# Kernel optimization log

Measured on AMD Instinct MI355X. Metric: run time of the kernel, lower is better.

The kernel has to match this reference:

```python
import jax, jax.numpy as jnp
import numpy as np

NUM_CLASSES = 80
STRIDES = (8, 16, 32)


def bce_logits(x, t):
    # numerically stable BCEWithLogits, reduction='none'
    return jnp.maximum(x, 0.) - x * t + jnp.log1p(jnp.exp(-jnp.abs(x)))


def decode_level(feat, stride):
    # feat: [B, C, H, W] -> decoded [B, HW, C], grid x/y [HW], strides [HW]
    B, C, H, W = feat.shape
    out = feat.reshape(B, C, H * W).transpose(0, 2, 1)  # [B, HW, C]
    yv, xv = jnp.meshgrid(jnp.arange(H), jnp.arange(W), indexing='ij')
    grid = jnp.stack([xv, yv], axis=-1).reshape(-1, 2).astype(feat.dtype)  # [HW, 2]
    xy = (out[..., :2] + grid[None]) * stride
    wh = jnp.exp(out[..., 2:4]) * stride
    out = jnp.concatenate([xy, wh, out[..., 4:]], axis=-1)
    return out, grid[:, 0], grid[:, 1], jnp.full((H * W,), float(stride), feat.dtype)


def pairwise_iou_cxcywh(g, p):
    # g: [G,4] gt boxes, p: [A,4] pred boxes (cx,cy,w,h) -> [G,A]
    tl = jnp.maximum(g[:, None, :2] - g[:, None, 2:] * 0.5, p[None, :, :2] - p[None, :, 2:] * 0.5)
    br = jnp.minimum(g[:, None, :2] + g[:, None, 2:] * 0.5, p[None, :, :2] + p[None, :, 2:] * 0.5)
    area_g = g[:, 2] * g[:, 3]
    area_p = p[:, 2] * p[:, 3]
    en = jnp.all(tl < br, axis=-1)
    inter = jnp.prod(br - tl, axis=-1) * en
    return inter / (area_g[:, None] + area_p[None, :] - inter + 1e-16)


def simota_assign(gt_boxes, gt_cls, bbox_p, cls_p, obj_p, xc, yc, strides):
    # per-image SimOTA label assignment (masked, jit-friendly)
    # gt_boxes [G,4], gt_cls [G] int, bbox_p [A,4], cls_p [A,C], obj_p [A,1]
    G = gt_boxes.shape[0]
    A = bbox_p.shape[0]
    gl = gt_boxes[:, 0:1] - 0.5 * gt_boxes[:, 2:3]
    gr = gt_boxes[:, 0:1] + 0.5 * gt_boxes[:, 2:3]
    gt_ = gt_boxes[:, 1:2] - 0.5 * gt_boxes[:, 3:4]
    gb = gt_boxes[:, 1:2] + 0.5 * gt_boxes[:, 3:4]
    in_box = (xc[None] > gl) & (xc[None] < gr) & (yc[None] > gt_) & (yc[None] < gb)  # [G,A]
    r = 2.5 * strides[None]
    in_ctr = ((xc[None] > gt_boxes[:, 0:1] - r) & (xc[None] < gt_boxes[:, 0:1] + r)
              & (yc[None] > gt_boxes[:, 1:2] - r) & (yc[None] < gt_boxes[:, 1:2] + r))
    geom = in_box | in_ctr
    anchor_ok = jnp.any(geom, axis=0)        # fg_mask candidate anchors [A]
    in_both = in_box & in_ctr                # [G,A]

    ious = pairwise_iou_cxcywh(gt_boxes, bbox_p)            # [G,A]
    ious = jnp.where(anchor_ok[None], ious, 0.)
    iou_cost = -jnp.log(ious + 1e-8)

    eps = 1e-8
    p = jnp.sqrt(jax.nn.sigmoid(cls_p) * jax.nn.sigmoid(obj_p))  # [A,C]
    logp = jnp.log(p + eps)
    log1mp = jnp.log(1. - p + eps)
    base = -jnp.sum(log1mp, axis=-1)                              # [A]
    sel = (logp - log1mp)[:, gt_cls]                              # [A,G]
    cls_cost = base[None, :] - sel.T                              # [G,A] = BCE(p, onehot).sum(-1)

    cost = cls_cost + 3.0 * iou_cost + 100000.0 * (~in_both) + 1e9 * (~anchor_ok[None])

    n_cand = min(10, A)
    topk_ious = jax.lax.top_k(ious, n_cand)[0]                    # [G,10]
    dyn_k = jnp.maximum(jnp.sum(topk_ious, axis=1).astype(jnp.int32), 1)  # [G]
    rank = jnp.argsort(jnp.argsort(cost, axis=1), axis=1)         # rank of each anchor per gt
    matching = (rank < dyn_k[:, None]) & anchor_ok[None]          # [G,A] bool

    am = jnp.sum(matching, axis=0)                                # anchors matched to >1 gt
    argmin_g = jnp.argmin(cost, axis=0)                           # [A]
    best = jnp.arange(G)[:, None] == argmin_g[None]               # [G,A]
    matching = jnp.where(am[None] > 1, best, matching)

    fg = jnp.any(matching, axis=0)                                # [A]
    matched_gt = jnp.argmax(matching, axis=0)                     # [A]
    pred_iou = jnp.sum(matching * ious, axis=0)                   # [A]
    cls_t = jax.nn.one_hot(gt_cls[matched_gt], NUM_CLASSES, dtype=bbox_p.dtype) * pred_iou[:, None]
    reg_t = gt_boxes[matched_gt]                                  # [A,4]
    return fg, cls_t, reg_t


def iou_elem(p, t):
    # elementwise IoU between matched pred/target boxes (cxcywh), IOUloss 'iou'
    tl = jnp.maximum(p[..., :2] - p[..., 2:] * 0.5, t[..., :2] - t[..., 2:] * 0.5)
    br = jnp.minimum(p[..., :2] + p[..., 2:] * 0.5, t[..., :2] + t[..., 2:] * 0.5)
    ap = p[..., 2] * p[..., 3]
    ag = t[..., 2] * t[..., 3]
    en = jnp.all(tl < br, axis=-1).astype(p.dtype)
    ai = jnp.prod(br - tl, axis=-1) * en
    return ai / (ap + ag - ai + 1e-16)


def yolo_loss(feat8, feat16, feat32, labels):
    outs, xs, ys, ss = [], [], [], []
    for feat, s in zip((feat8, feat16, feat32), STRIDES):
        o, x, y, st = decode_level(feat, s)
        outs.append(o); xs.append(x); ys.append(y); ss.append(st)
    outputs = jnp.concatenate(outs, axis=1)            # [B, A, 5+C]
    x_shifts = jnp.concatenate(xs)
    y_shifts = jnp.concatenate(ys)
    strides = jnp.concatenate(ss)
    xc = (x_shifts + 0.5) * strides                    # anchor centers [A]
    yc = (y_shifts + 0.5) * strides

    bbox_preds = outputs[..., :4]
    obj_preds = outputs[..., 4]
    cls_preds = outputs[..., 5:5 + NUM_CLASSES]

    labels_sg = jax.lax.stop_gradient(labels)
    gt_boxes = labels_sg[..., :4]
    gt_cls = labels_sg[..., 4].astype(jnp.int32)

    # assignment is @torch.no_grad in the original -> stop_gradient on its inputs
    fg, cls_t, reg_t = jax.vmap(simota_assign, in_axes=(0, 0, 0, 0, 0, None, None, None))(
        gt_boxes, gt_cls,
        jax.lax.stop_gradient(bbox_preds),
        jax.lax.stop_gradient(cls_preds),
        jax.lax.stop_gradient(outputs[..., 4:5]),
        xc, yc, strides)

    fg_f = fg.astype(outputs.dtype)                    # [B, A]
    iou = iou_elem(bbox_preds, reg_t)                  # [B, A]
    loss_iou = jnp.sum(fg_f * (1. - iou ** 2))
    loss_obj = jnp.sum(bce_logits(obj_preds, fg_f))
    loss_cls = jnp.sum(fg_f[..., None] * bce_logits(cls_preds, cls_t))
    num_fg = jnp.maximum(jnp.sum(fg_f), 1.)
    loss = (5.0 * loss_iou + 0.1 * loss_obj + loss_cls) / num_fg
    return loss


def setup_inputs() -> dict:
    key = jax.random.key(0)
    k1, k2, k3, k4, k5, k6, k7 = jax.random.split(key, 7)
    B, G = 32, 30
    feat8 = jax.random.normal(k1, (B, 85, 80, 80), jnp.float32)
    feat16 = jax.random.normal(k2, (B, 85, 40, 40), jnp.float32)
    feat32 = jax.random.normal(k3, (B, 85, 20, 20), jnp.float32)
    cx = jax.random.uniform(k4, (B, G, 1), jnp.float32, 60., 580.)
    cy = jax.random.uniform(k5, (B, G, 1), jnp.float32, 60., 580.)
    wh = jax.random.uniform(k6, (B, G, 2), jnp.float32, 20., 150.)
    cls = jax.random.randint(k7, (B, G, 1), 0, NUM_CLASSES).astype(jnp.float32)
    labels = jnp.concatenate([cx, cy, wh, cls], axis=-1)   # [B, G, 5] = cx,cy,w,h,cls
    return {"feat8": feat8, "feat16": feat16, "feat32": feat32, "labels": labels}


def reference(feat8, feat16, feat32, labels):
    return yolo_loss(feat8, feat16, feat32, labels)
```

## Files before the change

### kernel.cpp

```cpp
#include <hip/hip_runtime.h>
#include <cstdint>
#include <cstddef>

#define NB 32
#define NG 30
#define NA 8400
#define NC 80
#define SELB 512
#define MGRIDX 33
#define NBLK (MGRIDX * NB)
#define LCAP 128
#define DCAP 2304
#define NITER 17

typedef unsigned long long u64;

struct Params {
  const float* f8; const float* f16; const float* f32; const float* lab;
  float*    bbox;
  float*    objlog;
  float*    po;
  float*    base_;
  unsigned* gbits;
  unsigned* obits;
  unsigned* mmask;
  unsigned* dcount;
  unsigned* dlist;
  float*    part;
  float*    out;
};

__device__ __forceinline__ float fsigm(float x) {
  return __fdividef(1.0f, 1.0f + __expf(-x));
}

__device__ __forceinline__ void anchor_geom(int a, int& x, int& y, int& W, int& hw,
                                            float& stride, int& lvl) {
  if (a < 6400)      { W = 80; hw = 6400; stride = 8.f;  lvl = 0; int i = a;        y = i / 80; x = i - y * 80; }
  else if (a < 8000) { W = 40; hw = 1600; stride = 16.f; lvl = 1; int i = a - 6400; y = i / 40; x = i - y * 40; }
  else               { W = 20; hw = 400;  stride = 32.f; lvl = 2; int i = a - 8000; y = i / 20; x = i - y * 20; }
}

__device__ __forceinline__ float pair_iou(float px, float py, float pw, float ph,
                                          float glx, float gty, float grx, float gby,
                                          float area_g) {
  float tlx = fmaxf(glx, px - pw * 0.5f);
  float tly = fmaxf(gty, py - ph * 0.5f);
  float brx = fminf(grx, px + pw * 0.5f);
  float bry = fminf(gby, py + ph * 0.5f);
  float inter = ((tlx < brx) && (tly < bry)) ? (brx - tlx) * (bry - tly) : 0.0f;
  return __fdividef(inter, area_g + pw * ph - inter + 1e-16f);
}

__device__ __forceinline__ float cost_of(float4 pb, float po, float bs, unsigned gb,
                                         int g, float glx, float gty, float grx,
                                         float gby, float area_g, float xl,
                                         float& iou_out) {
  bool ok = (gb >> 31) & 1u;
  float iou = pair_iou(pb.x, pb.y, pb.z, pb.w, glx, gty, grx, gby, area_g);
  iou = ok ? iou : 0.0f;
  float iou_cost = -__logf(iou + 1e-8f);
  float pc = fsigm(xl);
  float pr = sqrtf(pc * po);
  float cls_cost = bs - (__logf(pr + 1e-8f) - __logf(1.0f - pr + 1e-8f));
  float c = cls_cost + 3.0f * iou_cost;
  c = c + (((gb >> g) & 1u) ? 0.0f : 100000.0f);
  c = c + (ok ? 0.0f : 1000000000.0f);
  iou_out = iou;
  return c;
}

__device__ __forceinline__ u64 packkey(float c, int a) {
  unsigned b = __float_as_uint(c);
  b = (b & 0x80000000u) ? ~b : (b | 0x80000000u);
  return ((u64)b << 32) | (unsigned)a;
}

__device__ float base_of(const Params& p, int b, int a, float po) {
  int lvl = (a < 6400) ? 0 : (a < 8000) ? 1 : 2;
  int hw  = (lvl == 0) ? 6400 : (lvl == 1) ? 1600 : 400;
  int loff = (lvl == 0) ? 0 : (lvl == 1) ? 6400 : 8000;
  const float* f = (lvl == 0) ? p.f8 : (lvl == 1) ? p.f16 : p.f32;
  int cb = b * 85 * hw + 5 * hw + (a - loff);
  float bs = 0.0f;
#pragma unroll 1
  for (int c = 0; c < NC; c++) {
    float xl = f[cb + c * hw];
    float pc = fsigm(xl);
    float pr = sqrtf(pc * po);
    bs -= __logf(1.0f - pr + 1e-8f);
  }
  return bs;
}

__global__ __launch_bounds__(256) void k_zero(Params p) {
  int i = threadIdx.x;
  if (i < NB) p.dcount[i] = 0u;
}

__global__ __launch_bounds__(256) void k_stage(Params p) {
  __shared__ float sgt[NG * 5];
  int b = blockIdx.y;
  int tid = threadIdx.x;
  if (tid < NG * 5) sgt[tid] = p.lab[b * NG * 5 + tid];
  __syncthreads();
  int a = blockIdx.x * 256 + tid;
  if (a >= NA) return;
  p.mmask[b * NA + a] = 0u;

  int x, y, W, hw, lvl; float stride;
  anchor_geom(a, x, y, W, hw, stride, lvl);
  const float* f = (lvl == 0) ? p.f8 : (lvl == 1) ? p.f16 : p.f32;
  int loff = (lvl == 0) ? 0 : (lvl == 1) ? 6400 : 8000;
  int fb = b * 85 * hw + (a - loff);

  float tx = f[fb];
  float ty = f[fb + hw];
  float tw = f[fb + 2 * hw];
  float th = f[fb + 3 * hw];
  float ob = f[fb + 4 * hw];

  float px = (tx + (float)x) * stride;
  float py = (ty + (float)y) * stride;
  float pw = __expf(tw) * stride;
  float ph = __expf(th) * stride;
  ((float4*)p.bbox)[b * NA + a] = make_float4(px, py, pw, ph);
  p.objlog[b * NA + a] = ob;
  p.po[b * NA + a] = fsigm(ob);

  float xc = ((float)x + 0.5f) * stride;
  float yc = ((float)y + 0.5f) * stride;
  float r = 2.5f * stride;
  float plx = px - 0.5f * pw, prx = px + 0.5f * pw;
  float pty = py - 0.5f * ph, pby = py + 0.5f * ph;
  unsigned gb = 0, ov = 0; int ok = 0;
#pragma unroll
  for (int g = 0; g < NG; g++) {
    float gx = sgt[g * 5], gy = sgt[g * 5 + 1], gw = sgt[g * 5 + 2], gh = sgt[g * 5 + 3];
    float glx = gx - 0.5f * gw, grx = gx + 0.5f * gw;
    float gty_ = gy - 0.5f * gh, gby = gy + 0.5f * gh;
    bool inb = (xc > glx) && (xc < grx) && (yc > gty_) && (yc < gby);
    bool inc = (xc > gx - r) && (xc < gx + r) && (yc > gy - r) && (yc < gy + r);
    ok |= (inb || inc) ? 1 : 0;
    gb |= (unsigned)(inb && inc) << g;
    bool o = (fmaxf(glx, plx) < fminf(grx, prx)) && (fmaxf(gty_, pty) < fminf(gby, pby));
    ov |= (unsigned)o << g;
  }
  gb |= (unsigned)ok << 31;
  p.gbits[b * NA + a] = gb;
  p.obits[b * NA + a] = ok ? ov : 0u;

  bool has = (gb & 0x3FFFFFFFu) != 0u;
  u64 bal = __ballot(has);
  if (bal) {
    int lane = tid & 63;
    int leader = __ffsll(bal) - 1;
    unsigned basec = 0;
    if (lane == leader) basec = atomicAdd(&p.dcount[b], (unsigned)__popcll(bal));
    basec = __shfl(basec, leader, 64);
    if (has) {
      unsigned s = basec + (unsigned)__popcll(bal & ((1ull << lane) - 1ull));
      if (s < DCAP) p.dlist[b * DCAP + s] = (unsigned)a;
    }
  }
}

__global__ __launch_bounds__(256) void k_base(Params p) {
  int b = blockIdx.y;
  unsigned n = p.dcount[b]; if (n > DCAP) n = DCAP;
  unsigned i = blockIdx.x * 256 + threadIdx.x;
  if (i >= n) return;
  int a = (int)p.dlist[b * DCAP + i];
  int lvl = (a < 6400) ? 0 : (a < 8000) ? 1 : 2;
  int hw  = (lvl == 0) ? 6400 : (lvl == 1) ? 1600 : 400;
  int loff = (lvl == 0) ? 0 : (lvl == 1) ? 6400 : 8000;
  const float* f = (lvl == 0) ? p.f8 : (lvl == 1) ? p.f16 : p.f32;
  int cb = b * 85 * hw + 5 * hw + (a - loff);
  float po = p.po[b * NA + a];
  float bs = 0.0f;
#pragma unroll 8
  for (int c = 0; c < NC; c++) {
    float xl = f[cb + c * hw];
    float pc = fsigm(xl);
    float pr = sqrtf(pc * po);
    bs -= __logf(1.0f - pr + 1e-8f);
  }
  p.base_[b * NA + a] = bs;
}

__device__ __forceinline__ u64 block_min_u64(u64 k, int tid, u64* swk) {
#pragma unroll
  for (int off = 32; off; off >>= 1) {
    u64 k2 = __shfl_down(k, off, 64);
    if (k2 < k) k = k2;
  }
  int wv = tid >> 6;
  if ((tid & 63) == 0) swk[wv] = k;
  __syncthreads();
  u64 m = swk[0];
#pragma unroll
  for (int w = 1; w < SELB / 64; w++) if (swk[w] < m) m = swk[w];
  __syncthreads();
  return m;
}

__global__ __launch_bounds__(SELB) void k_sel(Params p) {
  __shared__ float sh_iou[NA];
  __shared__ unsigned sh_cand[LCAP];
  __shared__ float swv[SELB / 64];
  __shared__ int   swi[SELB / 64];
  __shared__ u64   swk[SELB / 64];
  __shared__ int   sh_excl[10];
  __shared__ int   scnt, scand;
  int bg = blockIdx.x;
  int b = bg / NG, g = bg % NG;
  int tid = threadIdx.x;
  if (tid == 0) { scnt = 0; scand = 0; }

  const float* gt = p.lab + (b * NG + g) * 5;
  float gx = gt[0], gy = gt[1], gw = gt[2], gh = gt[3];
  int cg = (int)gt[4];
  float glx = gx - 0.5f * gw, grx = gx + 0.5f * gw;
  float gty = gy - 0.5f * gh, gby = gy + 0.5f * gh;
  float area_g = gw * gh;
  const float4*   bb  = (const float4*)p.bbox + b * NA;
  const unsigned* obv = p.obits + b * NA;
  const unsigned* gbv = p.gbits + b * NA;
  __syncthreads();

  int lane = tid & 63;
  for (int it = 0; it < NITER; it++) {
    int a = it * SELB + tid;
    unsigned ob = 0u, gbw = 0u;
    if (a < NA) { ob = obv[a]; gbw = gbv[a]; }
    bool act = (ob >> g) & 1u;
    bool cnd = (gbw >> g) & 1u;
    u64 bal = __ballot(act);
    if (bal) {
      int leader = __ffsll(bal) - 1;
      int basec = 0;
      if (lane == leader) basec = atomicAdd(&scnt, __popcll(bal));
      basec = __shfl(basec, leader, 64);
      if (act) {
        int pre = __popcll(bal & ((1ull << lane) - 1ull));
        float4 pb = bb[a];
        float iou = pair_iou(pb.x, pb.y, pb.z, pb.w, glx, gty, grx, gby, area_g);
        sh_iou[basec + pre] = iou;
      }
    }
    u64 bc = __ballot(cnd);
    if (bc) {
      int leader = __ffsll(bc) - 1;
      int basec = 0;
      if (lane == leader) basec = atomicAdd(&scand, __popcll(bc));
      basec = __shfl(basec, leader, 64);
      if (cnd) {
        int s = basec + __popcll(bc & ((1ull << lane) - 1ull));
        if (s < LCAP) sh_cand[s] = (unsigned)a;
      }
    }
  }
  __syncthreads();
  int n = scnt;

  float sum = 0.0f;
  for (int rnd = 0; rnd < 10; rnd++) {
    float mv = -1.0f; int mi = -1;
    for (int j = tid; j < n; j += SELB) {
      float v = sh_iou[j];
      if (v > mv) { mv = v; mi = j; }
    }
#pragma unroll
    for (int off = 32; off; off >>= 1) {
      float v2 = __shfl_down(mv, off, 64);
      int   i2 = __shfl_down(mi, off, 64);
      if (v2 > mv) { mv = v2; mi = i2; }
    }
    if ((tid & 63) == 0) { swv[tid >> 6] = mv; swi[tid >> 6] = mi; }
    __syncthreads();
    float bv = swv[0]; int bi = swi[0];
#pragma unroll
    for (int w = 1; w < SELB / 64; w++)
      if (swv[w] > bv) { bv = swv[w]; bi = swi[w]; }
    sum += fmaxf(bv, 0.0f);
    if (tid == 0 && bi >= 0) sh_iou[bi] = -1.0f;
    __syncthreads();
  }
  int dynk = (int)sum;
  if (dynk < 1) dynk = 1;

  int nc = scand; if (nc > LCAP) nc = LCAP;
  u64 key = ~0ull;
  if (tid < nc) {
    int a = (int)sh_cand[tid];
    float4 pb = bb[a];
    float po_ = p.po[b * NA + a];
    float bs_ = p.base_[b * NA + a];
    unsigned gb_ = gbv[a];
    int lvl = (a < 6400) ? 0 : (a < 8000) ? 1 : 2;
    int hw  = (lvl == 0) ? 6400 : (lvl == 1) ? 1600 : 400;
    int loff = (lvl == 0) ? 0 : (lvl == 1) ? 6400 : 8000;
    const float* f = (lvl == 0) ? p.f8 : (lvl == 1) ? p.f16 : p.f32;
    float xl = f[b * 85 * hw + (5 + cg) * hw + (a - loff)];
    float iou_;
    float c = cost_of(pb, po_, bs_, gb_, g, glx, gty, grx, gby, area_g, xl, iou_);
    key = packkey(c, a);
  }
  unsigned* mrow = p.mmask + b * NA;
  unsigned gbit = 1u << g;
  int matched = 0;
  for (int it = 0; it < dynk; it++) {
    u64 win = block_min_u64(key, tid, swk);
    if (win == ~0ull) break;
    if (key == win) {
      atomicOr(&mrow[(unsigned)(win & 0xFFFFFFFFu)], gbit);
      key = ~0ull;
    }
    matched++;
  }

  if (matched < dynk) {
    const float* pov = p.po + b * NA;
    for (int it = matched; it < dynk; it++) {
      u64 best = ~0ull;
      for (int al = tid; al < NA; al += SELB) {
        unsigned gb = gbv[al];
        if (!(gb >> 31)) continue;
        if ((gb >> g) & 1u) continue;
        bool skip = false;
        for (int e = matched; e < it; e++) if (sh_excl[e] == al) skip = true;
        if (skip) continue;
        float po_ = pov[al];
        float bs = base_of(p, b, al, po_);
        int lvl = (al < 6400) ? 0 : (al < 8000) ? 1 : 2;
        int hw  = (lvl == 0) ? 6400 : (lvl == 1) ? 1600 : 400;
        int loff = (lvl == 0) ? 0 : (lvl == 1) ? 6400 : 8000;
        const float* f = (lvl == 0) ? p.f8 : (lvl == 1) ? p.f16 : p.f32;
        float xl = f[b * 85 * hw + (5 + cg) * hw + (al - loff)];
        float4 pb = bb[al];
        float iou_;
        float c = cost_of(pb, po_, bs, gb, g, glx, gty, grx, gby, area_g, xl, iou_);
        u64 nk = packkey(c, al);
        if (nk < best) best = nk;
      }
      u64 win = block_min_u64(best, tid, swk);
      if (win == ~0ull) break;
      int aw = (int)(win & 0xFFFFFFFFu);
      if (best == win) {
        atomicOr(&mrow[aw], gbit);
        p.base_[b * NA + aw] = base_of(p, b, aw, pov[aw]);
      }
      if (tid == 0) sh_excl[it] = aw;
      __syncthreads();
    }
  }
}

__device__ __forceinline__ float block_sum(float val, volatile float* sw) {
#pragma unroll
  for (int off = 32; off > 0; off >>= 1) val += __shfl_down(val, off, 64);
  int lane = threadIdx.x & 63, wv = threadIdx.x >> 6;
  __syncthreads();
  if (lane == 0) sw[wv] = val;
  __syncthreads();
  float r = 0.0f;
  if (threadIdx.x == 0) r = sw[0] + sw[1] + sw[2] + sw[3];
  return r;
}

__global__ __launch_bounds__(256) void k_match(Params p) {
  __shared__ float sred[4];
  int b = blockIdx.y;
  int tid = threadIdx.x;
  int lane = tid & 63;
  int a = blockIdx.x * 256 + tid;
  bool valid = a < NA;

  float l_iou = 0.0f, l_obj = 0.0f, l_cls = 0.0f, l_nfg = 0.0f;
  unsigned mask = 0; int am = 0;
  bool fg = false; float pred_iou = 0.0f; int cg_ = 0;

  if (valid) {
    mask = p.mmask[b * NA + a];
    am = __popc(mask);
    fg = (mask != 0u);
    float ol = p.objlog[b * NA + a];
    float tfg = fg ? 1.0f : 0.0f;
    l_obj = fmaxf(ol, 0.0f) - ol * tfg + __logf(1.0f + __expf(-fabsf(ol)));
  }

  unsigned long long amb = __ballot(valid && am > 1);
  while (amb) {
    int src = __ffsll(amb) - 1;
    amb &= amb - 1ull;
    int aa = __shfl(a, src, 64);
    float4 pb = ((const float4*)p.bbox)[b * NA + aa];
    float po_ = p.po[b * NA + aa];
    float bs_ = p.base_[b * NA + aa];
    unsigned gb_ = p.gbits[b * NA + aa];

    int lvl = (aa < 6400) ? 0 : (aa < 8000) ? 1 : 2;
    int hw  = (lvl == 0) ? 6400 : (lvl == 1) ? 1600 : 400;
    int loff = (lvl == 0) ? 0 : (lvl == 1) ? 6400 : 8000;
    const float* f = (lvl == 0) ? p.f8 : (lvl == 1) ? p.f16 : p.f32;
    int cb = b * 85 * hw + 5 * hw + (aa - loff);

    float c = 3.4e38f; int gg = 0x7FFFFFFF;
    if (lane < NG) {
      const float* gtg = p.lab + (b * NG + lane) * 5;
      float gx = gtg[0], gy = gtg[1], gw = gtg[2], gh = gtg[3];
      int cg = (int)gtg[4];
      float xl = f[cb + cg * hw];
      float iou_;
      c = cost_of(pb, po_, bs_, gb_, lane,
                  gx - 0.5f * gw, gy - 0.5f * gh,
                  gx + 0.5f * gw, gy + 0.5f * gh, gw * gh, xl, iou_);
      gg = lane;
    }
#pragma unroll
    for (int off = 32; off; off >>= 1) {
      float c2 = __shfl_down(c, off, 64);
      int   g2 = __shfl_down(gg, off, 64);
      if (c2 < c || (c2 == c && g2 < gg)) { c = c2; gg = g2; }
    }
    gg = __shfl(gg, 0, 64);
    if (lane == src) mask = 1u << gg;
  }

  if (valid && fg) {
    l_nfg = 1.0f;
    int mg = __ffs(mask) - 1;
    const float* gtm = p.lab + (b * NG + mg) * 5;
    float gx = gtm[0], gy = gtm[1], gw = gtm[2], gh = gtm[3];
    cg_ = (int)gtm[4];
    float4 pb = ((const float4*)p.bbox)[b * NA + a];
    float iou = pair_iou(pb.x, pb.y, pb.z, pb.w,
                         gx - 0.5f * gw, gy - 0.5f * gh,
                         gx + 0.5f * gw, gy + 0.5f * gh, gw * gh);
    pred_iou = iou;
    l_iou = 1.0f - iou * iou;
  }

  unsigned long long fgb = __ballot(valid && fg);
  while (fgb) {
    int src = __ffsll(fgb) - 1;
    fgb &= fgb - 1ull;
    int   aa   = __shfl(a, src, 64);
    float piou = __shfl(pred_iou, src, 64);
    int   ccg  = __shfl(cg_, src, 64);

    int lvl = (aa < 6400) ? 0 : (aa < 8000) ? 1 : 2;
    int hw  = (lvl == 0) ? 6400 : (lvl == 1) ? 1600 : 400;
    int loff = (lvl == 0) ? 0 : (lvl == 1) ? 6400 : 8000;
    const float* f = (lvl == 0) ? p.f8 : (lvl == 1) ? p.f16 : p.f32;
    int cb = b * 85 * hw + 5 * hw + (aa - loff);

    float part = 0.0f;
#pragma unroll
    for (int c0 = 0; c0 < NC; c0 += 64) {
      int c = c0 + lane;
      if (c < NC) {
        float xl = f[cb + c * hw];
        float t = (c == ccg) ? piou : 0.0f;
        part += fmaxf(xl, 0.0f) - xl * t + __logf(1.0f + __expf(-fabsf(xl)));
      }
    }
#pragma unroll
    for (int off = 32; off; off >>= 1) part += __shfl_down(part, off, 64);
    if (lane == 0) l_cls += part;
  }

  float s0 = block_sum(l_iou, sred);
  float s1 = block_sum(l_obj, sred);
  float s2 = block_sum(l_cls, sred);
  float s3 = block_sum(l_nfg, sred);
  if (tid == 0) {
    ((float4*)p.part)[b * MGRIDX + blockIdx.x] = make_float4(s0, s1, s2, s3);
  }
}

__global__ __launch_bounds__(256) void k_final(Params p) {
  __shared__ float sred[4];
  int tid = threadIdx.x;
  float s0 = 0.0f, s1 = 0.0f, s2 = 0.0f, s3 = 0.0f;
  for (int i = tid; i < NBLK; i += 256) {
    float4 v = ((const float4*)p.part)[i];
    s0 += v.x; s1 += v.y; s2 += v.z; s3 += v.w;
  }
  s0 = block_sum(s0, sred);
  s1 = block_sum(s1, sred);
  s2 = block_sum(s2, sred);
  s3 = block_sum(s3, sred);
  if (tid == 0) {
    p.out[0] = (5.0f * s0 + 0.1f * s1 + s2) / fmaxf(s3, 1.0f);
  }
}

extern "C" void kernel_launch(void* const* d_in, const int* in_sizes, int n_in,
                              void* d_out, int out_size, void* d_ws, size_t ws_size,
                              hipStream_t stream) {
  Params p;
  p.f8  = (const float*)d_in[0];
  p.f16 = (const float*)d_in[1];
  p.f32 = (const float*)d_in[2];
  p.lab = (const float*)d_in[3];

  float* w = (float*)d_ws;
  p.bbox   = w;              w += (size_t)NB * NA * 4;
  p.objlog = w;              w += (size_t)NB * NA;
  p.po     = w;              w += (size_t)NB * NA;
  p.base_  = w;              w += (size_t)NB * NA;
  p.gbits  = (unsigned*)w;   w += (size_t)NB * NA;
  p.obits  = (unsigned*)w;   w += (size_t)NB * NA;
  p.mmask  = (unsigned*)w;   w += (size_t)NB * NA;
  p.dcount = (unsigned*)w;   w += (size_t)NB;
  p.dlist  = (unsigned*)w;   w += (size_t)NB * DCAP;
  p.part   = w;              w += (size_t)NBLK * 4;
  p.out    = (float*)d_out;

  dim3 gd(MGRIDX, NB);
  k_zero <<<1, 256, 0, stream>>>(p);
  k_stage<<<gd, 256, 0, stream>>>(p);
  k_base <<<dim3(DCAP / 256, NB), 256, 0, stream>>>(p);
  k_sel  <<<NB * NG, SELB, 0, stream>>>(p);
  k_match<<<gd, 256, 0, stream>>>(p);
  k_final<<<1, 256, 0, stream>>>(p);
}
```

Measured before the change: 204.1 us.

## Fuse base cost computation into staging kernel and drop compaction list

Removes the k_zero and k_base kernels and the atomic compaction list of candidate anchors. Each thread in k_stage now computes the 80-class base cost inline for its own anchor when it overlaps any gt in both box and center, reusing the sigmoid of the objectness it already holds. GT box edges are also precomputed once per block into shared arrays. This saves two launches and the list indirection, but the class loop now runs divergently inside a wave, since only some lanes take the branch.

```diff
diff --git a/kernel.cpp b/kernel.cpp
--- a/kernel.cpp
+++ b/kernel.cpp
@@ -10,7 +10,6 @@
 #define MGRIDX 33
 #define NBLK (MGRIDX * NB)
 #define LCAP 128
-#define DCAP 2304
 #define NITER 17
 
 typedef unsigned long long u64;
@@ -24,8 +23,6 @@
   unsigned* gbits;
   unsigned* obits;
   unsigned* mmask;
-  unsigned* dcount;
-  unsigned* dlist;
   float*    part;
   float*    out;
 };
@@ -93,16 +90,17 @@
   return bs;
 }
 
-__global__ __launch_bounds__(256) void k_zero(Params p) {
-  int i = threadIdx.x;
-  if (i < NB) p.dcount[i] = 0u;
-}
-
 __global__ __launch_bounds__(256) void k_stage(Params p) {
-  __shared__ float sgt[NG * 5];
+  __shared__ float sglx[NG], sgrx[NG], sgty[NG], sgby[NG], sgx[NG], sgy[NG];
   int b = blockIdx.y;
   int tid = threadIdx.x;
-  if (tid < NG * 5) sgt[tid] = p.lab[b * NG * 5 + tid];
+  if (tid < NG) {
+    const float* gt = p.lab + (b * NG + tid) * 5;
+    float gx = gt[0], gy = gt[1], gw = gt[2], gh = gt[3];
+    sgx[tid] = gx; sgy[tid] = gy;
+    sglx[tid] = gx - 0.5f * gw; sgrx[tid] = gx + 0.5f * gw;
+    sgty[tid] = gy - 0.5f * gh; sgby[tid] = gy + 0.5f * gh;
+  }
   __syncthreads();
   int a = blockIdx.x * 256 + tid;
   if (a >= NA) return;
@@ -126,7 +124,8 @@
   float ph = __expf(th) * stride;
   ((float4*)p.bbox)[b * NA + a] = make_float4(px, py, pw, ph);
   p.objlog[b * NA + a] = ob;
-  p.po[b * NA + a] = fsigm(ob);
+  float po_r = fsigm(ob);
+  p.po[b * NA + a] = po_r;
 
   float xc = ((float)x + 0.5f) * stride;
   float yc = ((float)y + 0.5f) * stride;
@@ -136,9 +135,8 @@
   unsigned gb = 0, ov = 0; int ok = 0;
 #pragma unroll
   for (int g = 0; g < NG; g++) {
-    float gx = sgt[g * 5], gy = sgt[g * 5 + 1], gw = sgt[g * 5 + 2], gh = sgt[g * 5 + 3];
-    float glx = gx - 0.5f * gw, grx = gx + 0.5f * gw;
-    float gty_ = gy - 0.5f * gh, gby = gy + 0.5f * gh;
+    float glx = sglx[g], grx = sgrx[g], gty_ = sgty[g], gby = sgby[g];
+    float gx = sgx[g], gy = sgy[g];
     bool inb = (xc > glx) && (xc < grx) && (yc > gty_) && (yc < gby);
     bool inc = (xc > gx - r) && (xc < gx + r) && (yc > gy - r) && (yc < gy + r);
     ok |= (inb || inc) ? 1 : 0;
@@ -150,42 +148,18 @@
   p.gbits[b * NA + a] = gb;
   p.obits[b * NA + a] = ok ? ov : 0u;
 
-  bool has = (gb & 0x3FFFFFFFu) != 0u;
-  u64 bal = __ballot(has);
-  if (bal) {
-    int lane = tid & 63;
-    int leader = __ffsll(bal) - 1;
-    unsigned basec = 0;
-    if (lane == leader) basec = atomicAdd(&p.dcount[b], (unsigned)__popcll(bal));
-    basec = __shfl(basec, leader, 64);
-    if (has) {
-      unsigned s = basec + (unsigned)__popcll(bal & ((1ull << lane) - 1ull));
-      if (s < DCAP) p.dlist[b * DCAP + s] = (unsigned)a;
-    }
-  }
-}
-
-__global__ __launch_bounds__(256) void k_base(Params p) {
-  int b = blockIdx.y;
-  unsigned n = p.dcount[b]; if (n > DCAP) n = DCAP;
-  unsigned i = blockIdx.x * 256 + threadIdx.x;
-  if (i >= n) return;
-  int a = (int)p.dlist[b * DCAP + i];
-  int lvl = (a < 6400) ? 0 : (a < 8000) ? 1 : 2;
-  int hw  = (lvl == 0) ? 6400 : (lvl == 1) ? 1600 : 400;
-  int loff = (lvl == 0) ? 0 : (lvl == 1) ? 6400 : 8000;
-  const float* f = (lvl == 0) ? p.f8 : (lvl == 1) ? p.f16 : p.f32;
-  int cb = b * 85 * hw + 5 * hw + (a - loff);
-  float po = p.po[b * NA + a];
-  float bs = 0.0f;
+  if (gb & 0x3FFFFFFFu) {
+    int cb = fb + 5 * hw;
+    float bs = 0.0f;
 #pragma unroll 8
-  for (int c = 0; c < NC; c++) {
-    float xl = f[cb + c * hw];
-    float pc = fsigm(xl);
-    float pr = sqrtf(pc * po);
-    bs -= __logf(1.0f - pr + 1e-8f);
-  }
-  p.base_[b * NA + a] = bs;
+    for (int c = 0; c < NC; c++) {
+      float xl = f[cb + c * hw];
+      float pc = fsigm(xl);
+      float pr = sqrtf(pc * po_r);
+      bs -= __logf(1.0f - pr + 1e-8f);
+    }
+    p.base_[b * NA + a] = bs;
+  }
 }
 
 __device__ __forceinline__ u64 block_min_u64(u64 k, int tid, u64* swk) {
@@ -513,15 +487,11 @@
   p.gbits  = (unsigned*)w;   w += (size_t)NB * NA;
   p.obits  = (unsigned*)w;   w += (size_t)NB * NA;
   p.mmask  = (unsigned*)w;   w += (size_t)NB * NA;
-  p.dcount = (unsigned*)w;   w += (size_t)NB;
-  p.dlist  = (unsigned*)w;   w += (size_t)NB * DCAP;
   p.part   = w;              w += (size_t)NBLK * 4;
   p.out    = (float*)d_out;
 
   dim3 gd(MGRIDX, NB);
-  k_zero <<<1, 256, 0, stream>>>(p);
   k_stage<<<gd, 256, 0, stream>>>(p);
-  k_base <<<dim3(DCAP / 256, NB), 256, 0, stream>>>(p);
   k_sel  <<<NB * NG, SELB, 0, stream>>>(p);
   k_match<<<gd, 256, 0, stream>>>(p);
   k_final<<<1, 256, 0, stream>>>(p);
```

Result: faster. 190.2 us (-6.8%).
